# Kernel tuning notes

Measured on AMD Instinct MI355X. Metric: run time of the kernel, lower is better.

## Reference

```python
import jax, jax.numpy as jnp
import numpy as np

B, L, DIM = 16, 2048, 256
EXPAND, D_STATE, D_CONV = 2, 16, 4
D_INNER = EXPAND * DIM
DT_RANK = (DIM + 15) // 16  # ceil(dim/16) = 16
MLP_HIDDEN = 512
LN_EPS = 1e-5


def silu(v):
    return v * jax.nn.sigmoid(v)


def layernorm(v, w, b):
    mu = jnp.mean(v, axis=-1, keepdims=True)
    var = jnp.mean(jnp.square(v - mu), axis=-1, keepdims=True)
    return (v - mu) * jax.lax.rsqrt(var + LN_EPS) * w + b


def ssm_branch(xz, conv_w, conv_b, xproj_w, dtproj_w, dtproj_b, A_log, D):
    # xz: (B, L, 2*d_inner) -> one directional Mamba branch (conv + silu + selective scan + gate)
    xh, z = jnp.split(xz, 2, axis=-1)
    # depthwise causal conv1d, kernel 4, left pad 3 (output truncated to L)
    xc = jnp.transpose(xh, (0, 2, 1))  # (B, d_inner, L)
    xc = jax.lax.conv_general_dilated(xc, conv_w, (1,), [(D_CONV - 1, 0)],
                                      feature_group_count=D_INNER)
    xc = xc + conv_b[None, :, None]
    xs = silu(jnp.transpose(xc, (0, 2, 1)))  # (B, L, d_inner)
    proj = xs @ xproj_w.T  # (B, L, dt_rank + 2*d_state)
    dt, Bm, Cm = jnp.split(proj, [DT_RANK, DT_RANK + D_STATE], axis=-1)
    dt = jax.nn.softplus(dt @ dtproj_w.T + dtproj_b)  # (B, L, d_inner)
    A = -jnp.exp(A_log)  # (d_inner, d_state)

    def step(h, inp):
        dt_t, B_t, C_t, x_t = inp  # (B,d), (B,n), (B,n), (B,d)
        dA = jnp.exp(dt_t[:, :, None] * A)  # (B, d, n)
        h = h * dA + (dt_t * x_t)[:, :, None] * B_t[:, None, :]
        y_t = jnp.einsum('bdn,bn->bd', h, C_t)
        return h, y_t

    h0 = jnp.zeros((xs.shape[0], D_INNER, D_STATE), xs.dtype)
    seq = (jnp.transpose(dt, (1, 0, 2)), jnp.transpose(Bm, (1, 0, 2)),
           jnp.transpose(Cm, (1, 0, 2)), jnp.transpose(xs, (1, 0, 2)))
    _, ys = jax.lax.scan(step, h0, seq)  # ys: (L, B, d_inner)
    y = jnp.transpose(ys, (1, 0, 2)) + xs * D
    return y * silu(z)


def setup_inputs() -> dict:
    key = jax.random.key(0)
    ks = jax.random.split(key, 16)
    nrm = lambda k, shape, s=0.02: jax.random.normal(k, shape, jnp.float32) * s
    A_log = jnp.log(jnp.broadcast_to(
        jnp.arange(1, D_STATE + 1, dtype=jnp.float32), (D_INNER, D_STATE)))
    return {
        'x': jax.random.normal(ks[0], (B, L, DIM), jnp.float32),
        'ln1_w': jnp.ones((DIM,), jnp.float32), 'ln1_b': jnp.zeros((DIM,), jnp.float32),
        'in_proj_w': nrm(ks[1], (2 * D_INNER, DIM)),
        'conv_w_f': nrm(ks[2], (D_INNER, 1, D_CONV), 0.1), 'conv_b_f': jnp.zeros((D_INNER,), jnp.float32),
        'xproj_w_f': nrm(ks[3], (DT_RANK + 2 * D_STATE, D_INNER)),
        'dtproj_w_f': nrm(ks[4], (D_INNER, DT_RANK), 0.1), 'dtproj_b_f': nrm(ks[5], (D_INNER,), 0.1),
        'A_log_f': A_log, 'D_f': jnp.ones((D_INNER,), jnp.float32),
        'conv_w_b': nrm(ks[6], (D_INNER, 1, D_CONV), 0.1), 'conv_b_b': jnp.zeros((D_INNER,), jnp.float32),
        'xproj_w_b': nrm(ks[7], (DT_RANK + 2 * D_STATE, D_INNER)),
        'dtproj_w_b': nrm(ks[8], (D_INNER, DT_RANK), 0.1), 'dtproj_b_b': nrm(ks[9], (D_INNER,), 0.1),
        'A_log_b': A_log, 'D_b': jnp.ones((D_INNER,), jnp.float32),
        'out_proj_w': nrm(ks[10], (DIM, D_INNER)),
        'ln2_w': jnp.ones((DIM,), jnp.float32), 'ln2_b': jnp.zeros((DIM,), jnp.float32),
        'fc1_w': nrm(ks[11], (MLP_HIDDEN, DIM)), 'fc1_b': jnp.zeros((MLP_HIDDEN,), jnp.float32),
        'fc2_w': nrm(ks[12], (DIM, MLP_HIDDEN)), 'fc2_b': jnp.zeros((DIM,), jnp.float32),
    }


def reference(x, ln1_w, ln1_b, in_proj_w,
              conv_w_f, conv_b_f, xproj_w_f, dtproj_w_f, dtproj_b_f, A_log_f, D_f,
              conv_w_b, conv_b_b, xproj_w_b, dtproj_w_b, dtproj_b_b, A_log_b, D_b,
              out_proj_w, ln2_w, ln2_b, fc1_w, fc1_b, fc2_w, fc2_b):
    # x = x + bimamba_v2(LN1(x))
    h = layernorm(x, ln1_w, ln1_b)
    xz = h @ in_proj_w.T  # (B, L, 2*d_inner)
    y_f = ssm_branch(xz, conv_w_f, conv_b_f, xproj_w_f, dtproj_w_f, dtproj_b_f, A_log_f, D_f)
    y_b = jnp.flip(ssm_branch(jnp.flip(xz, axis=1), conv_w_b, conv_b_b, xproj_w_b,
                              dtproj_w_b, dtproj_b_b, A_log_b, D_b), axis=1)
    x = x + ((y_f + y_b) * 0.5) @ out_proj_w.T  # if_divide_out=True -> /2
    # x = x + MLP(LN2(x))
    h2 = layernorm(x, ln2_w, ln2_b)
    m = jax.nn.gelu(h2 @ fc1_w.T + fc1_b, approximate=False) @ fc2_w.T + fc2_b
    return x + m
```

## Files before the change

### kernel.cpp

```cpp
#include <hip/hip_runtime.h>
#include <math.h>

#define LL 2048
#define NB 16
#define DMODEL 256
#define DIN 512
#define NCH 64
#define CLN (LL/NCH)
#define MROWS (NB*LL)
#define PLD 64

typedef unsigned short bf16_t;
typedef __bf16 bf16x8 __attribute__((ext_vector_type(8)));
typedef float f32x4 __attribute__((ext_vector_type(4)));
typedef float f32x2 __attribute__((ext_vector_type(2)));
typedef unsigned short u16x8 __attribute__((ext_vector_type(8)));

__device__ __forceinline__ float sigmoidf_(float x){ return 1.f/(1.f+__expf(-x)); }
__device__ __forceinline__ float siluf_(float x){ return x*sigmoidf_(x); }
__device__ __forceinline__ float softplusf_(float x){ return fmaxf(x,0.f) + __logf(1.f + __expf(-fabsf(x))); }
__device__ __forceinline__ float geluf_(float x){ return 0.5f*x*(1.f+erff(x*0.70710678118654752f)); }

__device__ __forceinline__ float bf2f(bf16_t u){
    union{unsigned int i; float f;} v; v.i = ((unsigned int)u)<<16; return v.f;
}
__device__ __forceinline__ bf16_t f2bf(float f){
    union{float f; unsigned int i;} v; v.f=f;
    unsigned int r = v.i + 0x7fffu + ((v.i>>16)&1u);
    return (bf16_t)(r>>16);
}

__device__ __forceinline__ void gl_lds16(const bf16_t* g, bf16_t* l){
    __builtin_amdgcn_global_load_lds(
        (const __attribute__((address_space(1))) void*)g,
        (__attribute__((address_space(3))) void*)l, 16, 0, 0);
}

#define ECHAINP(e1v, dA2) \
    f32x2 dA2[8]; { \
    float _e2=(e1v)*(e1v); \
    dA2[0]=(f32x2){(e1v),_e2}; \
    f32x2 _p={_e2,_e2}; \
    dA2[1]=dA2[0]*_p; dA2[2]=dA2[1]*_p; dA2[3]=dA2[2]*_p; \
    f32x2 _q={dA2[3].y,dA2[3].y}; \
    dA2[4]=dA2[0]*_q; dA2[5]=dA2[1]*_q; dA2[6]=dA2[2]*_q; dA2[7]=dA2[3]*_q; }

__global__ __launch_bounds__(256) void cvt_all(
    const float* __restrict__ ip, const float* __restrict__ op,
    const float* __restrict__ f1, const float* __restrict__ f2,
    const float* __restrict__ xf, const float* __restrict__ xb,
    bf16_t* __restrict__ w_ip, bf16_t* __restrict__ w_op,
    bf16_t* __restrict__ w_f1, bf16_t* __restrict__ w_f2,
    bf16_t* __restrict__ w_xf, bf16_t* __restrict__ w_xb)
{
    int blk = blockIdx.x, tid = threadIdx.x;
    const float* src; bf16_t* dst; int idx; int pad = 0;
    if(blk < 256){ src=ip; dst=w_ip; idx = blk*256+tid; }
    else if(blk < 384){ src=op; dst=w_op; idx=(blk-256)*256+tid; }
    else if(blk < 512){ src=f1; dst=w_f1; idx=(blk-384)*256+tid; }
    else if(blk < 640){ src=f2; dst=w_f2; idx=(blk-512)*256+tid; }
    else if(blk < 672){ src=xf; dst=w_xf; idx=(blk-640)*256+tid; pad=1; }
    else { src=xb; dst=w_xb; idx=(blk-672)*256+tid; pad=1; }
    int i4 = idx*4;
    ushort4 o;
    if(pad){
        int row = i4 >> 9;
        if(row < 48){
            float4 v = *(const float4*)(src + i4);
            o.x=f2bf(v.x); o.y=f2bf(v.y); o.z=f2bf(v.z); o.w=f2bf(v.w);
        } else o = make_ushort4(0,0,0,0);
    } else {
        float4 v = *(const float4*)(src + i4);
        o.x=f2bf(v.x); o.y=f2bf(v.y); o.z=f2bf(v.z); o.w=f2bf(v.w);
    }
    *(ushort4*)(dst + i4) = o;
}

__global__ __launch_bounds__(256) void ln_kernel(const float* __restrict__ X,
    const float* __restrict__ w, const float* __restrict__ b, bf16_t* __restrict__ O)
{
    int row = blockIdx.x*4 + (threadIdx.x>>6);
    int lane = threadIdx.x & 63;
    const float4 v = ((const float4*)(X + (size_t)row*DMODEL))[lane];
    float s = v.x+v.y+v.z+v.w;
    float s2 = v.x*v.x+v.y*v.y+v.z*v.z+v.w*v.w;
    #pragma unroll
    for(int o=32;o>0;o>>=1){ s += __shfl_xor(s,o); s2 += __shfl_xor(s2,o); }
    float mu = s*(1.f/DMODEL);
    float rs = rsqrtf(s2*(1.f/DMODEL)-mu*mu + 1e-5f);
    const float4 wv = ((const float4*)w)[lane];
    const float4 bv = ((const float4*)b)[lane];
    ushort4 o4;
    o4.x = f2bf((v.x-mu)*rs*wv.x+bv.x);
    o4.y = f2bf((v.y-mu)*rs*wv.y+bv.y);
    o4.z = f2bf((v.z-mu)*rs*wv.z+bv.z);
    o4.w = f2bf((v.w-mu)*rs*wv.w+bv.w);
    ((ushort4*)(O + (size_t)row*DMODEL))[lane] = o4;
}

template<int EPI, int BM, int BN>
__global__ __launch_bounds__(256) void mfma_gemm(
    const bf16_t* __restrict__ A, const bf16_t* __restrict__ W,
    float* Cf, bf16_t* Cb, bf16_t* C2b,
    const float* ADD, const float* __restrict__ BIAS,
    int N, int K)
{
    constexpr int WTM = BM/2, WTN = BN/2;
    constexpr int FM = WTM/16, FN = WTN/16;
    __shared__ alignas(16) bf16_t As[BM*32];
    __shared__ alignas(16) bf16_t Bs[BN*32];
    const int tid  = threadIdx.x;
    const int wid  = tid >> 6;
    const int lane = tid & 63;

    const int gx = gridDim.x, gy = gridDim.y;
    const int nwg = gx*gy;
    const int orig = blockIdx.y*gx + blockIdx.x;
    const int q = nwg>>3, r = nwg&7, xcd = orig&7, lin = orig>>3;
    const int wg = (xcd<r ? xcd*(q+1) : r*(q+1)+(xcd-r)*q) + lin;
    const int bx = wg / gy;
    const int by = wg - bx*gy;
    const int row0 = bx * BM;
    const int col0 = by * BN;

    const int srow  = (wid<<4) + (lane>>2);
    const int scolb = ((lane&3)<<4) ^ ((srow&3)<<4);
    const bf16_t* ga = A + (size_t)(row0+srow)*K + (scolb>>1);
    const bf16_t* gb = W + (size_t)(col0+srow)*K + (scolb>>1);
    bf16_t* la0 = As + (wid<<9);
    bf16_t* lb0 = Bs + (wid<<9);

    const int wr = wid>>1, wc = wid&1;
    const int l15 = lane&15, l4 = lane>>4;
    const int arow = wr*WTM + l15;
    const int brow = wc*WTN + l15;
    const int aoffe = arow*32 + ((l4<<3) ^ ((arow&3)<<3));
    const int boffe = brow*32 + ((l4<<3) ^ ((brow&3)<<3));

    f32x4 acc[FM][FN];
    #pragma unroll
    for(int i=0;i<FM;i++)
        #pragma unroll
        for(int j=0;j<FN;j++) acc[i][j] = (f32x4){0.f,0.f,0.f,0.f};

    for(int k0=0; k0<K; k0+=32){
        gl_lds16(ga, la0);
        if constexpr (BM==128) gl_lds16(ga + (size_t)64*K, As + 2048 + (wid<<9));
        gl_lds16(gb, lb0);
        if constexpr (BN==128) gl_lds16(gb + (size_t)64*K, Bs + 2048 + (wid<<9));
        ga += 32; gb += 32;
        __syncthreads();
        bf16x8 af[FM], bfr[FN];
        #pragma unroll
        for(int mi=0;mi<FM;mi++) af[mi]  = *(const bf16x8*)(As + aoffe + mi*512);
        #pragma unroll
        for(int ni=0;ni<FN;ni++) bfr[ni] = *(const bf16x8*)(Bs + boffe + ni*512);
        #pragma unroll
        for(int mi=0;mi<FM;mi++)
            #pragma unroll
            for(int ni=0;ni<FN;ni++)
                acc[mi][ni] = __builtin_amdgcn_mfma_f32_16x16x32_bf16(
                    af[mi], bfr[ni], acc[mi][ni], 0, 0, 0);
        __syncthreads();
    }

    const int orow0 = row0 + wr*WTM + (l4<<2);
    const int ocol0 = col0 + wc*WTN + l15;
    #pragma unroll
    for(int mi=0;mi<FM;mi++){
        #pragma unroll
        for(int rI=0;rI<4;rI++){
            int rr = orow0 + mi*16 + rI;
            #pragma unroll
            for(int ni=0;ni<FN;ni++){
                int cc = ocol0 + ni*16;
                float v = acc[mi][ni][rI];
                if(EPI==0){
                    if(cc < DIN) Cb [(size_t)rr*DIN + cc]        = f2bf(v);
                    else         C2b[(size_t)rr*DIN + cc - DIN]  = f2bf(v);
                } else if(EPI==1){
                    Cf[(size_t)rr*N + cc] = 0.5f*v + ADD[(size_t)rr*N + cc];
                } else if(EPI==2){
                    Cb[(size_t)rr*N + cc] = f2bf(geluf_(v + BIAS[cc]));
                } else if(EPI==3){
                    Cf[(size_t)rr*N + cc] = v + BIAS[cc] + ADD[(size_t)rr*N + cc];
                }
            }
        }
    }
}

__global__ __launch_bounds__(256) void xproj_pair(
    const bf16_t* __restrict__ Af, const bf16_t* __restrict__ Ab,
    const bf16_t* __restrict__ Wf, const bf16_t* __restrict__ Wb,
    float* __restrict__ Cfo, float* __restrict__ Cbo, int K)
{
    constexpr int BM=64, BN=64, WTM=32, WTN=32, FM=2, FN=2;
    __shared__ alignas(16) bf16_t As[BM*32];
    __shared__ alignas(16) bf16_t Bs[BN*32];
    const int tid  = threadIdx.x;
    const int wid  = tid >> 6;
    const int lane = tid & 63;

    const int gx = gridDim.x, gy = gridDim.y;
    const int nwg = gx*gy;
    const int orig = blockIdx.y*gx + blockIdx.x;
    const int q = nwg>>3, r = nwg&7, xcd = orig&7, lin = orig>>3;
    const int wg = (xcd<r ? xcd*(q+1) : r*(q+1)+(xcd-r)*q) + lin;
    const int bx = wg / gy;
    const int by = wg - bx*gy;
    const int row0 = bx * BM;
    const bf16_t* A = by ? Ab : Af;
    const bf16_t* W = by ? Wb : Wf;
    float* C = by ? Cbo : Cfo;

    const int srow  = (wid<<4) + (lane>>2);
    const int scolb = ((lane&3)<<4) ^ ((srow&3)<<4);
    const bf16_t* ga = A + (size_t)(row0+srow)*K + (scolb>>1);
    const bf16_t* gb = W + (size_t)srow*K + (scolb>>1);
    bf16_t* la0 = As + (wid<<9);
    bf16_t* lb0 = Bs + (wid<<9);

    const int wr = wid>>1, wc = wid&1;
    const int l15 = lane&15, l4 = lane>>4;
    const int arow = wr*WTM + l15;
    const int brow = wc*WTN + l15;
    const int aoffe = arow*32 + ((l4<<3) ^ ((arow&3)<<3));
    const int boffe = brow*32 + ((l4<<3) ^ ((brow&3)<<3));

    f32x4 acc[FM][FN];
    #pragma unroll
    for(int i=0;i<FM;i++)
        #pragma unroll
        for(int j=0;j<FN;j++) acc[i][j] = (f32x4){0.f,0.f,0.f,0.f};

    for(int k0=0; k0<K; k0+=32){
        gl_lds16(ga, la0);
        gl_lds16(gb, lb0);
        ga += 32; gb += 32;
        __syncthreads();
        bf16x8 af[FM], bfr[FN];
        #pragma unroll
        for(int mi=0;mi<FM;mi++) af[mi]  = *(const bf16x8*)(As + aoffe + mi*512);
        #pragma unroll
        for(int ni=0;ni<FN;ni++) bfr[ni] = *(const bf16x8*)(Bs + boffe + ni*512);
        #pragma unroll
        for(int mi=0;mi<FM;mi++)
            #pragma unroll
            for(int ni=0;ni<FN;ni++)
                acc[mi][ni] = __builtin_amdgcn_mfma_f32_16x16x32_bf16(
                    af[mi], bfr[ni], acc[mi][ni], 0, 0, 0);
        __syncthreads();
    }

    const int orow0 = row0 + wr*WTM + (l4<<2);
    const int ocol0 = wc*WTN + l15;
    #pragma unroll
    for(int mi=0;mi<FM;mi++)
        #pragma unroll
        for(int rI=0;rI<4;rI++){
            int rr = orow0 + mi*16 + rI;
            #pragma unroll
            for(int ni=0;ni<FN;ni++)
                C[(size_t)rr*PLD + ocol0 + ni*16] = acc[mi][ni][rI];
        }
}

__global__ __launch_bounds__(256) void conv_pair(const bf16_t* __restrict__ X,
    const float* __restrict__ cwf, const float* __restrict__ cbf,
    const float* __restrict__ cwb, const float* __restrict__ cbb,
    bf16_t* __restrict__ XSf, bf16_t* __restrict__ XSb)
{
    const int half = MROWS*DIN/32;
    int gid = blockIdx.x*256 + threadIdx.x;
    int rev = gid >= half; gid -= rev ? half : 0;
    const float* cw = rev ? cwb : cbf==nullptr?cwf:cwb, *cb_;
    cw = rev ? cwb : cwf; cb_ = rev ? cbb : cbf;
    bf16_t* XS = rev ? XSb : XSf;
    int d8 = gid & 63;
    int rest = gid >> 6;
    int t4 = rest & 511;
    int b  = rest >> 9;
    int t0 = t4 << 2;
    int d0 = d8 << 3;

    float w[8][4];
    #pragma unroll
    for(int dd=0; dd<8; dd++){
        float4 w4 = *(const float4*)(cw + (d0+dd)*4);
        w[dd][0]=w4.x; w[dd][1]=w4.y; w[dd][2]=w4.z; w[dd][3]=w4.w;
    }
    float bias[8];
    {
        float4 b0 = *(const float4*)(cb_ + d0);
        float4 b1 = *(const float4*)(cb_ + d0 + 4);
        bias[0]=b0.x; bias[1]=b0.y; bias[2]=b0.z; bias[3]=b0.w;
        bias[4]=b1.x; bias[5]=b1.y; bias[6]=b1.z; bias[7]=b1.w;
    }
    float rowf[7][8];
    #pragma unroll
    for(int jr=0; jr<7; jr++){
        int tt = t0 - 3 + jr;
        if(tt < 0){
            #pragma unroll
            for(int dd=0;dd<8;dd++) rowf[jr][dd] = 0.f;
        } else {
            int rr = rev ? (LL-1-tt) : tt;
            u16x8 rr8 = *(const u16x8*)(X + ((size_t)(b*LL + rr))*DIN + d0);
            #pragma unroll
            for(int dd=0;dd<8;dd++) rowf[jr][dd] = bf2f(rr8[dd]);
        }
    }
    #pragma unroll
    for(int k=0;k<4;k++){
        u16x8 o;
        #pragma unroll
        for(int dd=0;dd<8;dd++){
            float acc = bias[dd];
            #pragma unroll
            for(int j=0;j<4;j++) acc = fmaf(w[dd][j], rowf[k+j][dd], acc);
            __bf16 hb = (__bf16)siluf_(acc);
            o[dd] = __builtin_bit_cast(unsigned short, hb);
        }
        *(u16x8*)(XS + ((size_t)(b*LL) + t0 + k)*DIN + d0) = o;
    }
}

__global__ __launch_bounds__(512) void scanA_pair(
    const float* __restrict__ PROJf, const float* __restrict__ PROJb,
    const bf16_t* __restrict__ XSf, const bf16_t* __restrict__ XSb,
    const float* __restrict__ dtwf, const float* __restrict__ dtbf,
    const float* __restrict__ dtwb, const float* __restrict__ dtbb,
    float* __restrict__ SUMDTf, float* __restrict__ SUMDTb,
    _Float16* __restrict__ HENDf, _Float16* __restrict__ HENDb)
{
    __shared__ float Pl[CLN][32];
    int bx = blockIdx.x;
    int br = bx >= NB*NCH;
    int bc = bx - (br ? NB*NCH : 0);
    const float* PROJ = br ? PROJb : PROJf;
    const bf16_t* XS  = br ? XSb : XSf;
    const float* dtw  = br ? dtwb : dtwf;
    const float* dtb  = br ? dtbb : dtbf;
    float* SUMDT      = br ? SUMDTb : SUMDTf;
    _Float16* HEND    = br ? HENDb : HENDf;

    int d = threadIdx.x;
    size_t row0 = (size_t)bc*CLN;
    if(d < 256){
        int row = d >> 3, qq = d & 7;
        float4 v = *(const float4*)(PROJ + (row0+row)*PLD + qq*4);
        *(float4*)&Pl[row][qq*4] = v;
    }
    float w[16];
    #pragma unroll
    for(int r=0;r<4;r++){
        float4 a = *(const float4*)(dtw + d*16 + r*4);
        w[4*r]=a.x; w[4*r+1]=a.y; w[4*r+2]=a.z; w[4*r+3]=a.w;
    }
    float bv = dtb[d];
    f32x2 h[8];
    #pragma unroll
    for(int n=0;n<8;n++) h[n] = (f32x2){0.f,0.f};
    float sumdt = 0.f;
    const bf16_t* px = XS + row0*DIN + d;
    __syncthreads();
    #pragma unroll 2
    for(int t=0;t<CLN;t++){
        float a0 = bv;
        #pragma unroll
        for(int r=0;r<4;r++){
            float4 p4 = *(const float4*)&Pl[t][r*4];
            a0 = fmaf(p4.x,w[4*r],a0); a0 = fmaf(p4.y,w[4*r+1],a0);
            a0 = fmaf(p4.z,w[4*r+2],a0); a0 = fmaf(p4.w,w[4*r+3],a0);
        }
        float4 B0 = *(const float4*)&Pl[t][16];
        float4 B1 = *(const float4*)&Pl[t][20];
        float4 B2 = *(const float4*)&Pl[t][24];
        float4 B3 = *(const float4*)&Pl[t][28];
        float dt = softplusf_(a0);
        sumdt += dt;
        float xv = bf2f(*px); px += DIN;
        float e1 = __expf(-dt);
        float dtx = dt*xv;
        ECHAINP(e1, dA2)
        f32x2 dx = {dtx, dtx};
        h[0] = h[0]*dA2[0] + dx*(f32x2){B0.x,B0.y};
        h[1] = h[1]*dA2[1] + dx*(f32x2){B0.z,B0.w};
        h[2] = h[2]*dA2[2] + dx*(f32x2){B1.x,B1.y};
        h[3] = h[3]*dA2[3] + dx*(f32x2){B1.z,B1.w};
        h[4] = h[4]*dA2[4] + dx*(f32x2){B2.x,B2.y};
        h[5] = h[5]*dA2[5] + dx*(f32x2){B2.z,B2.w};
        h[6] = h[6]*dA2[6] + dx*(f32x2){B3.x,B3.y};
        h[7] = h[7]*dA2[7] + dx*(f32x2){B3.z,B3.w};
    }
    SUMDT[(size_t)bc*DIN + d] = sumdt;
    #pragma unroll
    for(int n=0;n<8;n++){
        HEND[((size_t)bc*16 + 2*n  )*DIN + d] = (_Float16)h[n].x;
        HEND[((size_t)bc*16 + 2*n+1)*DIN + d] = (_Float16)h[n].y;
    }
}

__global__ __launch_bounds__(256) void scan_fix_pair(
    const float* __restrict__ Alogf, const float* __restrict__ Alogb,
    const float* __restrict__ SUMDTf, const float* __restrict__ SUMDTb,
    _Float16* __restrict__ HENDf, _Float16* __restrict__ HENDb)
{
    const int half = (NB*DIN*16)/256;
    int blk = blockIdx.x;
    int br = blk >= half; blk -= br ? half : 0;
    const float* Alog = br ? Alogb : Alogf;
    const float* SUMDT = br ? SUMDTb : SUMDTf;
    _Float16* HEND = br ? HENDb : HENDf;
    int g = blk*256 + threadIdx.x;
    int d = g & (DIN-1);
    int n = (g>>9) & 15;
    int b = g >> 13;
    float Av = -__expf(Alog[d*16+n]);
    float carry = 0.f;
    for(int c=0;c<NCH;c++){
        size_t bc = (size_t)(b*NCH + c);
        float P = __expf(Av * SUMDT[bc*DIN + d]);
        size_t idx = (bc*16 + n)*DIN + d;
        float he = (float)HEND[idx];
        HEND[idx] = (_Float16)carry;
        carry = fmaf(P, carry, he);
    }
}

__global__ __launch_bounds__(256) void passC_bidir(
    const bf16_t* __restrict__ XSf, const bf16_t* __restrict__ XSb,
    const float* __restrict__ PROJf, const float* __restrict__ PROJb,
    const bf16_t* __restrict__ Z,
    const float* __restrict__ dtwf, const float* __restrict__ dtbf,
    const float* __restrict__ Dpf,
    const float* __restrict__ dtwb, const float* __restrict__ dtbb,
    const float* __restrict__ Dpb,
    const _Float16* __restrict__ HENDf, const _Float16* __restrict__ HENDb,
    bf16_t* __restrict__ YA)
{
    __shared__ float Plf[CLN][48];
    __shared__ float Plb[CLN][48];
    __shared__ _Float16 yf16[CLN][256];
    int blk = blockIdx.x;
    int dblk = blk & 1;
    int c = (blk>>1) & (NCH-1);
    int b = blk >> 7;
    int d = dblk*256 + threadIdx.x;
    int cb = NCH-1-c;
    size_t rowf = (size_t)b*LL + c*CLN;
    size_t rowb = (size_t)b*LL + cb*CLN;
    for(int i=threadIdx.x; i<CLN*12; i+=256){
        int row = i/12, qq = i-row*12;
        *(float4*)&Plf[row][qq*4] = *(const float4*)(PROJf + (rowf+row)*PLD + qq*4);
        *(float4*)&Plb[row][qq*4] = *(const float4*)(PROJb + (rowb+row)*PLD + qq*4);
    }
    __syncthreads();
    {
        float w[16];
        #pragma unroll
        for(int r=0;r<4;r++){
            float4 a = *(const float4*)(dtwf + d*16 + r*4);
            w[4*r]=a.x; w[4*r+1]=a.y; w[4*r+2]=a.z; w[4*r+3]=a.w;
        }
        float bv = dtbf[d], Dv = Dpf[d];
        size_t bc = (size_t)(b*NCH + c);
        f32x2 h[8];
        #pragma unroll
        for(int n=0;n<8;n++){
            h[n].x = (float)HENDf[(bc*16 + 2*n  )*DIN + d];
            h[n].y = (float)HENDf[(bc*16 + 2*n+1)*DIN + d];
        }
        const bf16_t* px = XSf + rowf*DIN + d;
        #pragma unroll 2
        for(int t=0;t<CLN;t++){
            float a0 = bv;
            #pragma unroll
            for(int r=0;r<4;r++){
                float4 p4 = *(const float4*)&Plf[t][r*4];
                a0 = fmaf(p4.x,w[4*r],a0); a0 = fmaf(p4.y,w[4*r+1],a0);
                a0 = fmaf(p4.z,w[4*r+2],a0); a0 = fmaf(p4.w,w[4*r+3],a0);
            }
            float4 Bq0 = *(const float4*)&Plf[t][16];
            float4 Bq1 = *(const float4*)&Plf[t][20];
            float4 Bq2 = *(const float4*)&Plf[t][24];
            float4 Bq3 = *(const float4*)&Plf[t][28];
            float4 Cq0 = *(const float4*)&Plf[t][32];
            float4 Cq1 = *(const float4*)&Plf[t][36];
            float4 Cq2 = *(const float4*)&Plf[t][40];
            float4 Cq3 = *(const float4*)&Plf[t][44];
            float dt = softplusf_(a0);
            float xv = bf2f(*px); px += DIN;
            float e1 = __expf(-dt);
            float dtx = dt*xv;
            ECHAINP(e1, dA2)
            f32x2 dx = {dtx, dtx};
            f32x2 y2 = {0.f, 0.f};
            h[0] = h[0]*dA2[0] + dx*(f32x2){Bq0.x,Bq0.y}; y2 = y2 + h[0]*(f32x2){Cq0.x,Cq0.y};
            h[1] = h[1]*dA2[1] + dx*(f32x2){Bq0.z,Bq0.w}; y2 = y2 + h[1]*(f32x2){Cq0.z,Cq0.w};
            h[2] = h[2]*dA2[2] + dx*(f32x2){Bq1.x,Bq1.y}; y2 = y2 + h[2]*(f32x2){Cq1.x,Cq1.y};
            h[3] = h[3]*dA2[3] + dx*(f32x2){Bq1.z,Bq1.w}; y2 = y2 + h[3]*(f32x2){Cq1.z,Cq1.w};
            h[4] = h[4]*dA2[4] + dx*(f32x2){Bq2.x,Bq2.y}; y2 = y2 + h[4]*(f32x2){Cq2.x,Cq2.y};
            h[5] = h[5]*dA2[5] + dx*(f32x2){Bq2.z,Bq2.w}; y2 = y2 + h[5]*(f32x2){Cq2.z,Cq2.w};
            h[6] = h[6]*dA2[6] + dx*(f32x2){Bq3.x,Bq3.y}; y2 = y2 + h[6]*(f32x2){Cq3.x,Cq3.y};
            h[7] = h[7]*dA2[7] + dx*(f32x2){Bq3.z,Bq3.w}; y2 = y2 + h[7]*(f32x2){Cq3.z,Cq3.w};
            yf16[t][threadIdx.x] = (_Float16)(y2.x + y2.y + xv*Dv);
        }
    }
    __syncthreads();
    {
        float w[16];
        #pragma unroll
        for(int r=0;r<4;r++){
            float4 a = *(const float4*)(dtwb + d*16 + r*4);
            w[4*r]=a.x; w[4*r+1]=a.y; w[4*r+2]=a.z; w[4*r+3]=a.w;
        }
        float bv = dtbb[d], Dv = Dpb[d];
        size_t bc = (size_t)(b*NCH + cb);
        f32x2 h[8];
        #pragma unroll
        for(int n=0;n<8;n++){
            h[n].x = (float)HENDb[(bc*16 + 2*n  )*DIN + d];
            h[n].y = (float)HENDb[(bc*16 + 2*n+1)*DIN + d];
        }
        const bf16_t* px = XSb + rowb*DIN + d;
        const bf16_t* pz = Z + (rowf + CLN-1)*DIN + d;
        bf16_t* py = YA + (rowf + CLN-1)*DIN + d;
        #pragma unroll 2
        for(int t=0;t<CLN;t++){
            float a0 = bv;
            #pragma unroll
            for(int r=0;r<4;r++){
                float4 p4 = *(const float4*)&Plb[t][r*4];
                a0 = fmaf(p4.x,w[4*r],a0); a0 = fmaf(p4.y,w[4*r+1],a0);
                a0 = fmaf(p4.z,w[4*r+2],a0); a0 = fmaf(p4.w,w[4*r+3],a0);
            }
            float4 Bq0 = *(const float4*)&Plb[t][16];
            float4 Bq1 = *(const float4*)&Plb[t][20];
            float4 Bq2 = *(const float4*)&Plb[t][24];
            float4 Bq3 = *(const float4*)&Plb[t][28];
            float4 Cq0 = *(const float4*)&Plb[t][32];
            float4 Cq1 = *(const float4*)&Plb[t][36];
            float4 Cq2 = *(const float4*)&Plb[t][40];
            float4 Cq3 = *(const float4*)&Plb[t][44];
            float dt = softplusf_(a0);
            float xv = bf2f(*px); px += DIN;
            float e1 = __expf(-dt);
            float dtx = dt*xv;
            ECHAINP(e1, dA2)
            f32x2 dx = {dtx, dtx};
            f32x2 y2 = {0.f, 0.f};
            h[0] = h[0]*dA2[0] + dx*(f32x2){Bq0.x,Bq0.y}; y2 = y2 + h[0]*(f32x2){Cq0.x,Cq0.y};
            h[1] = h[1]*dA2[1] + dx*(f32x2){Bq0.z,Bq0.w}; y2 = y2 + h[1]*(f32x2){Cq0.z,Cq0.w};
            h[2] = h[2]*dA2[2] + dx*(f32x2){Bq1.x,Bq1.y}; y2 = y2 + h[2]*(f32x2){Cq1.x,Cq1.y};
            h[3] = h[3]*dA2[3] + dx*(f32x2){Bq1.z,Bq1.w}; y2 = y2 + h[3]*(f32x2){Cq1.z,Cq1.w};
            h[4] = h[4]*dA2[4] + dx*(f32x2){Bq2.x,Bq2.y}; y2 = y2 + h[4]*(f32x2){Cq2.x,Cq2.y};
            h[5] = h[5]*dA2[5] + dx*(f32x2){Bq2.z,Bq2.w}; y2 = y2 + h[5]*(f32x2){Cq2.z,Cq2.w};
            h[6] = h[6]*dA2[6] + dx*(f32x2){Bq3.x,Bq3.y}; y2 = y2 + h[6]*(f32x2){Cq3.x,Cq3.y};
            h[7] = h[7]*dA2[7] + dx*(f32x2){Bq3.z,Bq3.w}; y2 = y2 + h[7]*(f32x2){Cq3.z,Cq3.w};
            float tot = (y2.x + y2.y + xv*Dv) + (float)yf16[CLN-1-t][threadIdx.x];
            float zv = bf2f(*pz); pz -= DIN;
            *py = f2bf(tot * siluf_(zv)); py -= DIN;
        }
    }
}

extern "C" void kernel_launch(void* const* d_in, const int* in_sizes, int n_in,
                              void* d_out, int out_size, void* d_ws, size_t ws_size,
                              hipStream_t stream) {
    const float* x        = (const float*)d_in[0];
    const float* ln1_w    = (const float*)d_in[1];
    const float* ln1_b    = (const float*)d_in[2];
    const float* in_proj  = (const float*)d_in[3];
    const float* conv_w_f = (const float*)d_in[4];
    const float* conv_b_f = (const float*)d_in[5];
    const float* xproj_f  = (const float*)d_in[6];
    const float* dtw_f    = (const float*)d_in[7];
    const float* dtb_f    = (const float*)d_in[8];
    const float* Alog_f   = (const float*)d_in[9];
    const float* D_f      = (const float*)d_in[10];
    const float* conv_w_b = (const float*)d_in[11];
    const float* conv_b_b = (const float*)d_in[12];
    const float* xproj_b  = (const float*)d_in[13];
    const float* dtw_b    = (const float*)d_in[14];
    const float* dtb_b    = (const float*)d_in[15];
    const float* Alog_b   = (const float*)d_in[16];
    const float* D_b      = (const float*)d_in[17];
    const float* out_proj = (const float*)d_in[18];
    const float* ln2_w    = (const float*)d_in[19];
    const float* ln2_b    = (const float*)d_in[20];
    const float* fc1_w    = (const float*)d_in[21];
    const float* fc1_b    = (const float*)d_in[22];
    const float* fc2_w    = (const float*)d_in[23];
    const float* fc2_b    = (const float*)d_in[24];
    float* out = (float*)d_out;

    bf16_t* X     = (bf16_t*)d_ws;
    bf16_t* Zb    = X   + (size_t)MROWS*DIN;
    bf16_t* XSf   = Zb  + (size_t)MROWS*DIN;
    bf16_t* XSb   = XSf + (size_t)MROWS*DIN;
    float*  PROJf = (float*)(XSb + (size_t)MROWS*DIN);
    float*  PROJb = PROJf + (size_t)MROWS*PLD;
    bf16_t* YA    = (bf16_t*)(PROJb + (size_t)MROWS*PLD);
    bf16_t* H     = YA;
    float*  SUMDTf= (float*)(YA + (size_t)MROWS*DIN);
    float*  SUMDTb= SUMDTf + (size_t)NB*NCH*DIN;
    _Float16* HENDf = (_Float16*)(SUMDTb + (size_t)NB*NCH*DIN);
    _Float16* HENDb = HENDf + (size_t)NB*NCH*DIN*16;
    bf16_t* w_ip = (bf16_t*)(HENDb + (size_t)NB*NCH*DIN*16);
    bf16_t* w_op = w_ip + 1024*256;
    bf16_t* w_f1 = w_op + 256*512;
    bf16_t* w_f2 = w_f1 + 512*256;
    bf16_t* w_xf = w_f2 + 256*512;
    bf16_t* w_xb = w_xf + 64*512;
    bf16_t* MBUF = XSf;

    dim3 blk(256);

    cvt_all<<<704, blk, 0, stream>>>(in_proj, out_proj, fc1_w, fc2_w,
        xproj_f, xproj_b, w_ip, w_op, w_f1, w_f2, w_xf, w_xb);

    ln_kernel<<<MROWS/4, blk, 0, stream>>>(x, ln1_w, ln1_b, H);
    mfma_gemm<0,128,128><<<dim3(MROWS/128, 1024/128), blk, 0, stream>>>(
        H, w_ip, nullptr, X, Zb, nullptr, nullptr, 1024, DMODEL);

    conv_pair<<<(MROWS*DIN/32)/256*2, blk, 0, stream>>>(X,
        conv_w_f, conv_b_f, conv_w_b, conv_b_b, XSf, XSb);
    xproj_pair<<<dim3(MROWS/64, 2), blk, 0, stream>>>(
        XSf, XSb, w_xf, w_xb, PROJf, PROJb, DIN);
    scanA_pair<<<NB*NCH*2, dim3(512), 0, stream>>>(PROJf, PROJb, XSf, XSb,
        dtw_f, dtb_f, dtw_b, dtb_b, SUMDTf, SUMDTb, HENDf, HENDb);
    scan_fix_pair<<<(NB*DIN*16)/256*2, blk, 0, stream>>>(
        Alog_f, Alog_b, SUMDTf, SUMDTb, HENDf, HENDb);
    passC_bidir<<<NB*NCH*2, blk, 0, stream>>>(XSf, XSb, PROJf, PROJb, Zb,
        dtw_f, dtb_f, D_f, dtw_b, dtb_b, D_b, HENDf, HENDb, YA);

    mfma_gemm<1,64,64><<<dim3(MROWS/64, DMODEL/64), blk, 0, stream>>>(
        YA, w_op, out, nullptr, nullptr, x, nullptr, DMODEL, DIN);
    ln_kernel<<<MROWS/4, blk, 0, stream>>>(out, ln2_w, ln2_b, H);
    mfma_gemm<2,64,64><<<dim3(MROWS/64, 512/64), blk, 0, stream>>>(
        H, w_f1, nullptr, MBUF, nullptr, nullptr, fc1_b, 512, DMODEL);
    mfma_gemm<3,64,64><<<dim3(MROWS/64, DMODEL/64), blk, 0, stream>>>(
        MBUF, w_f2, out, nullptr, nullptr, out, fc2_b, DMODEL, 512);
}
```

Baseline: 372.1 us.

## Cache softplus dt in fp16 from scanA and reuse in passC; keep forward y in registers

scanA now writes the per-step dt (after softplus) as fp16 into buffers aliased onto X and the output. passC reads these instead of recomputing the 16-term dt projection and softplus, so it only stages B and C in shared memory. The forward-direction outputs are kept in a register array instead of an fp16 shared-memory tile, which removes a syncthreads. The trade-off is extra global writes and reads of dt, fp16 rounding of dt, and higher register pressure from the fully unrolled 32-entry array.

```diff
diff --git a/kernel.cpp b/kernel.cpp
--- a/kernel.cpp
+++ b/kernel.cpp
@@ -274,8 +274,8 @@
     const int half = MROWS*DIN/32;
     int gid = blockIdx.x*256 + threadIdx.x;
     int rev = gid >= half; gid -= rev ? half : 0;
-    const float* cw = rev ? cwb : cbf==nullptr?cwf:cwb, *cb_;
-    cw = rev ? cwb : cwf; cb_ = rev ? cbb : cbf;
+    const float* cw = rev ? cwb : cwf;
+    const float* cb_ = rev ? cbb : cbf;
     bf16_t* XS = rev ? XSb : XSf;
     int d8 = gid & 63;
     int rest = gid >> 6;
@@ -331,6 +331,7 @@
     const bf16_t* __restrict__ XSf, const bf16_t* __restrict__ XSb,
     const float* __restrict__ dtwf, const float* __restrict__ dtbf,
     const float* __restrict__ dtwb, const float* __restrict__ dtbb,
+    _Float16* __restrict__ DTf, _Float16* __restrict__ DTb,
     float* __restrict__ SUMDTf, float* __restrict__ SUMDTb,
     _Float16* __restrict__ HENDf, _Float16* __restrict__ HENDb)
 {
@@ -342,6 +343,7 @@
     const bf16_t* XS  = br ? XSb : XSf;
     const float* dtw  = br ? dtwb : dtwf;
     const float* dtb  = br ? dtbb : dtbf;
+    _Float16* DT      = br ? DTb : DTf;
     float* SUMDT      = br ? SUMDTb : SUMDTf;
     _Float16* HEND    = br ? HENDb : HENDf;
 
@@ -364,6 +366,7 @@
     for(int n=0;n<8;n++) h[n] = (f32x2){0.f,0.f};
     float sumdt = 0.f;
     const bf16_t* px = XS + row0*DIN + d;
+    _Float16* pdt = DT + row0*DIN + d;
     __syncthreads();
     #pragma unroll 2
     for(int t=0;t<CLN;t++){
@@ -380,6 +383,7 @@
         float4 B3 = *(const float4*)&Pl[t][28];
         float dt = softplusf_(a0);
         sumdt += dt;
+        *pdt = (_Float16)dt; pdt += DIN;
         float xv = bf2f(*px); px += DIN;
         float e1 = __expf(-dt);
         float dtx = dt*xv;
@@ -433,16 +437,13 @@
     const bf16_t* __restrict__ XSf, const bf16_t* __restrict__ XSb,
     const float* __restrict__ PROJf, const float* __restrict__ PROJb,
     const bf16_t* __restrict__ Z,
-    const float* __restrict__ dtwf, const float* __restrict__ dtbf,
-    const float* __restrict__ Dpf,
-    const float* __restrict__ dtwb, const float* __restrict__ dtbb,
-    const float* __restrict__ Dpb,
+    const _Float16* __restrict__ DTf, const _Float16* __restrict__ DTb,
+    const float* __restrict__ Dpf, const float* __restrict__ Dpb,
     const _Float16* __restrict__ HENDf, const _Float16* __restrict__ HENDb,
     bf16_t* __restrict__ YA)
 {
-    __shared__ float Plf[CLN][48];
-    __shared__ float Plb[CLN][48];
-    __shared__ _Float16 yf16[CLN][256];
+    __shared__ float Plf[CLN][32];
+    __shared__ float Plb[CLN][32];
     int blk = blockIdx.x;
     int dblk = blk & 1;
     int c = (blk>>1) & (NCH-1);
@@ -451,20 +452,15 @@
     int cb = NCH-1-c;
     size_t rowf = (size_t)b*LL + c*CLN;
     size_t rowb = (size_t)b*LL + cb*CLN;
-    for(int i=threadIdx.x; i<CLN*12; i+=256){
-        int row = i/12, qq = i-row*12;
-        *(float4*)&Plf[row][qq*4] = *(const float4*)(PROJf + (rowf+row)*PLD + qq*4);
-        *(float4*)&Plb[row][qq*4] = *(const float4*)(PROJb + (rowb+row)*PLD + qq*4);
+    {
+        int row = threadIdx.x >> 3, qq = threadIdx.x & 7;
+        *(float4*)&Plf[row][qq*4] = *(const float4*)(PROJf + (rowf+row)*PLD + 16 + qq*4);
+        *(float4*)&Plb[row][qq*4] = *(const float4*)(PROJb + (rowb+row)*PLD + 16 + qq*4);
     }
     __syncthreads();
+    float yfr[CLN];
     {
-        float w[16];
-        #pragma unroll
-        for(int r=0;r<4;r++){
-            float4 a = *(const float4*)(dtwf + d*16 + r*4);
-            w[4*r]=a.x; w[4*r+1]=a.y; w[4*r+2]=a.z; w[4*r+3]=a.w;
-        }
-        float bv = dtbf[d], Dv = Dpf[d];
+        float Dv = Dpf[d];
         size_t bc = (size_t)(b*NCH + c);
         f32x2 h[8];
         #pragma unroll
@@ -473,50 +469,30 @@
             h[n].y = (float)HENDf[(bc*16 + 2*n+1)*DIN + d];
         }
         const bf16_t* px = XSf + rowf*DIN + d;
-        #pragma unroll 2
+        const _Float16* pdt = DTf + rowf*DIN + d;
+        #pragma unroll
         for(int t=0;t<CLN;t++){
-            float a0 = bv;
-            #pragma unroll
-            for(int r=0;r<4;r++){
-                float4 p4 = *(const float4*)&Plf[t][r*4];
-                a0 = fmaf(p4.x,w[4*r],a0); a0 = fmaf(p4.y,w[4*r+1],a0);
-                a0 = fmaf(p4.z,w[4*r+2],a0); a0 = fmaf(p4.w,w[4*r+3],a0);
-            }
-            float4 Bq0 = *(const float4*)&Plf[t][16];
-            float4 Bq1 = *(const float4*)&Plf[t][20];
-            float4 Bq2 = *(const float4*)&Plf[t][24];
-            float4 Bq3 = *(const float4*)&Plf[t][28];
-            float4 Cq0 = *(const float4*)&Plf[t][32];
-            float4 Cq1 = *(const float4*)&Plf[t][36];
-            float4 Cq2 = *(const float4*)&Plf[t][40];
-            float4 Cq3 = *(const float4*)&Plf[t][44];
-            float dt = softplusf_(a0);
+            float dt = (float)*pdt; pdt += DIN;
             float xv = bf2f(*px); px += DIN;
             float e1 = __expf(-dt);
             float dtx = dt*xv;
             ECHAINP(e1, dA2)
             f32x2 dx = {dtx, dtx};
             f32x2 y2 = {0.f, 0.f};
-            h[0] = h[0]*dA2[0] + dx*(f32x2){Bq0.x,Bq0.y}; y2 = y2 + h[0]*(f32x2){Cq0.x,Cq0.y};
-            h[1] = h[1]*dA2[1] + dx*(f32x2){Bq0.z,Bq0.w}; y2 = y2 + h[1]*(f32x2){Cq0.z,Cq0.w};
-            h[2] = h[2]*dA2[2] + dx*(f32x2){Bq1.x,Bq1.y}; y2 = y2 + h[2]*(f32x2){Cq1.x,Cq1.y};
-            h[3] = h[3]*dA2[3] + dx*(f32x2){Bq1.z,Bq1.w}; y2 = y2 + h[3]*(f32x2){Cq1.z,Cq1.w};
-            h[4] = h[4]*dA2[4] + dx*(f32x2){Bq2.x,Bq2.y}; y2 = y2 + h[4]*(f32x2){Cq2.x,Cq2.y};
-            h[5] = h[5]*dA2[5] + dx*(f32x2){Bq2.z,Bq2.w}; y2 = y2 + h[5]*(f32x2){Cq2.z,Cq2.w};
-            h[6] = h[6]*dA2[6] + dx*(f32x2){Bq3.x,Bq3.y}; y2 = y2 + h[6]*(f32x2){Cq3.x,Cq3.y};
-            h[7] = h[7]*dA2[7] + dx*(f32x2){Bq3.z,Bq3.w}; y2 = y2 + h[7]*(f32x2){Cq3.z,Cq3.w};
-            yf16[t][threadIdx.x] = (_Float16)(y2.x + y2.y + xv*Dv);
-        }
-    }
-    __syncthreads();
+            #pragma unroll
+            for(int n=0;n<4;n++){
+                float4 Bq = *(const float4*)&Plf[t][4*n];
+                float4 Cq = *(const float4*)&Plf[t][16+4*n];
+                h[2*n  ] = h[2*n  ]*dA2[2*n  ] + dx*(f32x2){Bq.x,Bq.y};
+                y2 = y2 + h[2*n  ]*(f32x2){Cq.x,Cq.y};
+                h[2*n+1] = h[2*n+1]*dA2[2*n+1] + dx*(f32x2){Bq.z,Bq.w};
+                y2 = y2 + h[2*n+1]*(f32x2){Cq.z,Cq.w};
+            }
+            yfr[t] = y2.x + y2.y + xv*Dv;
+        }
+    }
     {
-        float w[16];
-        #pragma unroll
-        for(int r=0;r<4;r++){
-            float4 a = *(const float4*)(dtwb + d*16 + r*4);
-            w[4*r]=a.x; w[4*r+1]=a.y; w[4*r+2]=a.z; w[4*r+3]=a.w;
-        }
-        float bv = dtbb[d], Dv = Dpb[d];
+        float Dv = Dpb[d];
         size_t bc = (size_t)(b*NCH + cb);
         f32x2 h[8];
         #pragma unroll
@@ -525,41 +501,28 @@
             h[n].y = (float)HENDb[(bc*16 + 2*n+1)*DIN + d];
         }
         const bf16_t* px = XSb + rowb*DIN + d;
+        const _Float16* pdt = DTb + rowb*DIN + d;
         const bf16_t* pz = Z + (rowf + CLN-1)*DIN + d;
         bf16_t* py = YA + (rowf + CLN-1)*DIN + d;
-        #pragma unroll 2
+        #pragma unroll
         for(int t=0;t<CLN;t++){
-            float a0 = bv;
-            #pragma unroll
-            for(int r=0;r<4;r++){
-                float4 p4 = *(const float4*)&Plb[t][r*4];
-                a0 = fmaf(p4.x,w[4*r],a0); a0 = fmaf(p4.y,w[4*r+1],a0);
-                a0 = fmaf(p4.z,w[4*r+2],a0); a0 = fmaf(p4.w,w[4*r+3],a0);
-            }
-            float4 Bq0 = *(const float4*)&Plb[t][16];
-            float4 Bq1 = *(const float4*)&Plb[t][20];
-            float4 Bq2 = *(const float4*)&Plb[t][24];
-            float4 Bq3 = *(const float4*)&Plb[t][28];
-            float4 Cq0 = *(const float4*)&Plb[t][32];
-            float4 Cq1 = *(const float4*)&Plb[t][36];
-            float4 Cq2 = *(const float4*)&Plb[t][40];
-            float4 Cq3 = *(const float4*)&Plb[t][44];
-            float dt = softplusf_(a0);
+            float dt = (float)*pdt; pdt += DIN;
             float xv = bf2f(*px); px += DIN;
             float e1 = __expf(-dt);
             float dtx = dt*xv;
             ECHAINP(e1, dA2)
             f32x2 dx = {dtx, dtx};
             f32x2 y2 = {0.f, 0.f};
-            h[0] = h[0]*dA2[0] + dx*(f32x2){Bq0.x,Bq0.y}; y2 = y2 + h[0]*(f32x2){Cq0.x,Cq0.y};
-            h[1] = h[1]*dA2[1] + dx*(f32x2){Bq0.z,Bq0.w}; y2 = y2 + h[1]*(f32x2){Cq0.z,Cq0.w};
-            h[2] = h[2]*dA2[2] + dx*(f32x2){Bq1.x,Bq1.y}; y2 = y2 + h[2]*(f32x2){Cq1.x,Cq1.y};
-            h[3] = h[3]*dA2[3] + dx*(f32x2){Bq1.z,Bq1.w}; y2 = y2 + h[3]*(f32x2){Cq1.z,Cq1.w};
-            h[4] = h[4]*dA2[4] + dx*(f32x2){Bq2.x,Bq2.y}; y2 = y2 + h[4]*(f32x2){Cq2.x,Cq2.y};
-            h[5] = h[5]*dA2[5] + dx*(f32x2){Bq2.z,Bq2.w}; y2 = y2 + h[5]*(f32x2){Cq2.z,Cq2.w};
-            h[6] = h[6]*dA2[6] + dx*(f32x2){Bq3.x,Bq3.y}; y2 = y2 + h[6]*(f32x2){Cq3.x,Cq3.y};
-            h[7] = h[7]*dA2[7] + dx*(f32x2){Bq3.z,Bq3.w}; y2 = y2 + h[7]*(f32x2){Cq3.z,Cq3.w};
-            float tot = (y2.x + y2.y + xv*Dv) + (float)yf16[CLN-1-t][threadIdx.x];
+            #pragma unroll
+            for(int n=0;n<4;n++){
+                float4 Bq = *(const float4*)&Plb[t][4*n];
+                float4 Cq = *(const float4*)&Plb[t][16+4*n];
+                h[2*n  ] = h[2*n  ]*dA2[2*n  ] + dx*(f32x2){Bq.x,Bq.y};
+                y2 = y2 + h[2*n  ]*(f32x2){Cq.x,Cq.y};
+                h[2*n+1] = h[2*n+1]*dA2[2*n+1] + dx*(f32x2){Bq.z,Bq.w};
+                y2 = y2 + h[2*n+1]*(f32x2){Cq.z,Cq.w};
+            }
+            float tot = (y2.x + y2.y + xv*Dv) + yfr[CLN-1-t];
             float zv = bf2f(*pz); pz -= DIN;
             *py = f2bf(tot * siluf_(zv)); py -= DIN;
         }
@@ -615,6 +578,8 @@
     bf16_t* w_xf = w_f2 + 256*512;
     bf16_t* w_xb = w_xf + 64*512;
     bf16_t* MBUF = XSf;
+    _Float16* DTf = (_Float16*)X;
+    _Float16* DTb = (_Float16*)out;
 
     dim3 blk(256);
 
@@ -630,11 +595,11 @@
     xproj_pair<<<dim3(MROWS/64, 2), blk, 0, stream>>>(
         XSf, XSb, w_xf, w_xb, PROJf, PROJb, DIN);
     scanA_pair<<<NB*NCH*2, dim3(512), 0, stream>>>(PROJf, PROJb, XSf, XSb,
-        dtw_f, dtb_f, dtw_b, dtb_b, SUMDTf, SUMDTb, HENDf, HENDb);
+        dtw_f, dtb_f, dtw_b, dtb_b, DTf, DTb, SUMDTf, SUMDTb, HENDf, HENDb);
     scan_fix_pair<<<(NB*DIN*16)/256*2, blk, 0, stream>>>(
         Alog_f, Alog_b, SUMDTf, SUMDTb, HENDf, HENDb);
     passC_bidir<<<NB*NCH*2, blk, 0, stream>>>(XSf, XSb, PROJf, PROJb, Zb,
-        dtw_f, dtb_f, D_f, dtw_b, dtb_b, D_b, HENDf, HENDb, YA);
+        DTf, DTb, D_f, D_b, HENDf, HENDb, YA);
 
     mfma_gemm<1,64,64><<<dim3(MROWS/64, DMODEL/64), blk, 0, stream>>>(
         YA, w_op, out, nullptr, nullptr, x, nullptr, DMODEL, DIN);
```

After: 350.1 us (median of 2 runs). 5.9% less time.
